# Kernel tuning notes

Hardware: AMD Instinct MI355X
Metric: run time of the kernel (lower is better)

Reference implementation:

```python
import jax, jax.numpy as jnp
import numpy as np
from jax import lax

B, S, F, H, O, U = 512, 168, 12, 128, 3, 256
PERIODS = (3, 6, 12, 24)


def _glorot(key, shape):
    fan_in = shape[-1]
    fan_out = shape[-2] if len(shape) >= 2 else shape[-1]
    scale = jnp.sqrt(2.0 / (fan_in + fan_out))
    return jax.random.normal(key, shape, jnp.float32) * scale


def setup_inputs() -> dict:
    key = jax.random.key(0)
    ks = iter(jax.random.split(key, 64))
    inp = {"x": jax.random.normal(next(ks), (B, 1, F, S), jnp.float32)}
    # 3 SFF groups (group1: enc_in=12, groups 2/3: enc_in=3) share conv/linear shapes per period
    for p in PERIODS:
        k = 1 + 2 * (p // 2)
        inp[f"conv{p}"] = _glorot(next(ks), (3, k))             # [group, kernel]
        inp[f"lin{p}"] = _glorot(next(ks), (3, S // p, S // p))  # [group, seg_y, seg_x]
    inp["Wb0"] = _glorot(next(ks), (U, F + H)); inp["bb0"] = jnp.zeros((U,), jnp.float32)
    inp["Wb1"] = _glorot(next(ks), (U, U));     inp["bb1"] = jnp.zeros((U,), jnp.float32)
    inp["Wff1"] = _glorot(next(ks), (H, U));    inp["bff1"] = jnp.zeros((H,), jnp.float32)
    inp["Wff2"] = _glorot(next(ks), (H, U));    inp["bff2"] = jnp.zeros((H,), jnp.float32)
    inp["Wta"] = _glorot(next(ks), (H, U));     inp["bta"] = jnp.zeros((H,), jnp.float32)
    inp["Wtb"] = _glorot(next(ks), (H, U));     inp["btb"] = jnp.zeros((H,), jnp.float32)
    inp["Wfc"] = _glorot(next(ks), (O, H));     inp["bfc"] = jnp.zeros((O,), jnp.float32)
    inp["Wfits"] = _glorot(next(ks), (O, S, S))  # FF: individual per-channel linear seq->pred
    return inp


def _sff(x, conv_w, lin_w, p):
    # x: [B, S, C]; conv_w: [k]; lin_w: [seg_y, seg_x]
    Bx, Sx, C = x.shape
    xp = jnp.transpose(x, (0, 2, 1))                      # [B, C, S]
    xr = xp.reshape(Bx * C, 1, Sx)
    pad = p // 2
    conv = lax.conv_general_dilated(xr, conv_w.reshape(1, 1, -1), (1,), [(pad, pad)],
                                    dimension_numbers=("NCH", "OIH", "NCH"))
    xc = conv.reshape(Bx, C, Sx) + xp                     # residual smoothing
    seg = Sx // p
    xc = jnp.transpose(xc.reshape(Bx * C, seg, p), (0, 2, 1))  # [B*C, p, seg_x]
    y = jnp.einsum("npk,qk->npq", xc, lin_w)              # [B*C, p, seg_y]
    y = jnp.transpose(y, (0, 2, 1)).reshape(Bx, C, -1)    # [B, C, pred]
    return jnp.transpose(y, (0, 2, 1))                    # [B, pred, C]


def reference(x, conv3, lin3, conv6, lin6, conv12, lin12, conv24, lin24,
              Wb0, bb0, Wb1, bb1, Wff1, bff1, Wff2, bff2,
              Wta, bta, Wtb, btb, Wfc, bfc, Wfits):
    convs = {3: conv3, 6: conv6, 12: conv12, 24: conv24}
    lins = {3: lin3, 6: lin6, 12: lin12, 24: lin24}

    xs = jnp.transpose(x[:, 0], (0, 2, 1))                # [B, S, F]
    seq_mean = jnp.mean(xs, axis=1, keepdims=True)        # [B, 1, F]
    xs = xs - seq_mean

    x1 = sum(_sff(xs, convs[p][0], lins[p][0], p) for p in PERIODS) * 0.25   # [B,S,F]
    xin3 = x1[:, :, :3]
    x2 = sum(_sff(xin3, convs[p][1], lins[p][1], p) for p in PERIODS) * 0.25  # [B,S,3]
    x3 = sum(_sff(xin3, convs[p][2], lins[p][2], p) for p in PERIODS) * 0.25  # [B,S,3]

    # CfC recurrence (ts == 1.0 everywhere; dropout in eval mode = identity)
    def step(h, xt):
        z = jnp.concatenate([xt, h], axis=1)
        z = jax.nn.silu(z @ Wb0.T + bb0)
        z = jax.nn.silu(z @ Wb1.T + bb1)
        ff1 = jnp.tanh(z @ Wff1.T + bff1)
        ff2 = jnp.tanh(z @ Wff2.T + bff2)
        t_interp = jax.nn.sigmoid((z @ Wta.T + bta) + (z @ Wtb.T + btb))
        h_new = ff1 * (1.0 - t_interp) + t_interp * ff2
        return h_new, h_new

    h0 = jnp.zeros((x1.shape[0], Wff1.shape[0]), x1.dtype)
    _, hs = lax.scan(step, h0, jnp.transpose(x1, (1, 0, 2)))  # hs: [S, B, H]

    readout = jnp.einsum("sbh,oh->bso", hs, Wfc) + bfc        # [B, S, O]
    readout = readout + x3
    readout = jnp.einsum("bsc,cps->bpc", readout, Wfits)      # FF (per-channel S -> pred)
    return readout + seq_mean[:, :, :3] + x2
```

## Files before the change

### kernel.cpp

```cpp
#include <hip/hip_runtime.h>

#define BB 512
#define SS 168
#define FF 12
#define HH 128
#define UU 256

typedef unsigned short u16;
typedef unsigned int   u32;
typedef _Float16 f16x8 __attribute__((ext_vector_type(8)));
typedef float    f32x4 __attribute__((ext_vector_type(4)));

__device__ __forceinline__ float sigmoidf_(float x){ return __fdividef(1.f, 1.f + __expf(-x)); }
__device__ __forceinline__ float siluf_(float x){ return x * sigmoidf_(x); }
__device__ __forceinline__ float tanhf_(float x){
    float t = __expf(-2.f * fabsf(x));
    float y = __fdividef(1.f - t, 1.f + t);
    return copysignf(y, x);
}
__device__ __forceinline__ u16 f2h_(float v){ return __builtin_bit_cast(u16, (_Float16)v); }
__device__ __forceinline__ f16x8 bc8_(uint4 v){ return __builtin_bit_cast(f16x8, v); }
__device__ __forceinline__ int aslot_(int row, int k){
    return (k >> 5) * 512 + ((k & 31) >> 3) * 128 + row * 8 + (k & 7);
}

#define MFMA16(a, b, acc) __builtin_amdgcn_mfma_f32_16x16x32_f16((a), (b), (acc), 0, 0, 0)

#define PREP_BLOCKS 810
#define SFFA_BLOCKS (BB * FF)

__global__ __launch_bounds__(256) void front_kernel(
    const float* __restrict__ x,
    const float* __restrict__ c3,  const float* __restrict__ l3,
    const float* __restrict__ c6,  const float* __restrict__ l6,
    const float* __restrict__ c12, const float* __restrict__ l12,
    const float* __restrict__ c24, const float* __restrict__ l24,
    const float* __restrict__ Wb0, const float* __restrict__ Wb1,
    const float* __restrict__ Wff1, const float* __restrict__ Wff2,
    const float* __restrict__ Wta, const float* __restrict__ Wtb,
    const float* __restrict__ Wfc,
    u16* __restrict__ W0f, u16* __restrict__ W1f, u16* __restrict__ W4f,
    float* __restrict__ meanbuf, float* __restrict__ x1,
    float* __restrict__ x2, float* __restrict__ x3)
{
    if (blockIdx.x < PREP_BLOCKS) {
        int t = blockIdx.x * 256 + threadIdx.x;
        if (t < 43520) {
            int e = t & 7, c = (t >> 3) & 15, g = (t >> 7) & 3, rest = t >> 9;
            int s = rest % 5, tt = rest / 5;
            int k = s * 32 + g * 8 + e;
            float v;
            if (tt < 16) { int u = tt * 16 + c; v = (k < 140) ? Wb0[u * 140 + k] : 0.f; }
            else         { v = (c < 3 && k >= 12 && k < 140) ? Wfc[c * 128 + (k - 12)] : 0.f; }
            W0f[t] = f2h_(v);
        } else if (t < 43520 + 65536) {
            int t1 = t - 43520;
            int e = t1 & 7, c = (t1 >> 3) & 15, g = (t1 >> 7) & 3, rest = t1 >> 9;
            int s = rest & 7, tt = rest >> 3;
            int u = tt * 16 + c, k = s * 32 + g * 8 + e;
            W1f[t1] = f2h_(Wb1[u * 256 + k]);
        } else if (t < 43520 + 65536 + 98304) {
            int t2 = t - 109056;
            int e = t2 & 7, c = (t2 >> 3) & 15, g = (t2 >> 7) & 3, rest = t2 >> 9;
            int s = rest & 7, tt = rest >> 3;
            int u = (tt & 7) * 16 + c, k = s * 32 + g * 8 + e;
            float v;
            if      (tt < 8)  v = Wff1[u * 256 + k];
            else if (tt < 16) v = Wff2[u * 256 + k];
            else              v = Wta[u * 256 + k] + Wtb[u * 256 + k];
            W4f[t2] = f2h_(v);
        }
        return;
    }

    int bc = blockIdx.x - PREP_BLOCKS;
    int b = bc / FF, c = bc % FF;
    __shared__ float v[SS], cv[SS], red[256];
    int tid = threadIdx.x;

    float raw = 0.f;
    if (tid < SS) raw = x[(b * FF + c) * SS + tid];
    red[tid] = raw;
    __syncthreads();
    for (int off = 128; off > 0; off >>= 1) {
        if (tid < off) red[tid] += red[tid + off];
        __syncthreads();
    }
    float mv = red[0] * (1.f / SS);
    if (tid == 0) meanbuf[b * FF + c] = mv;
    if (tid < SS) v[tid] = raw - mv;
    __syncthreads();

    const float* cw[4]  = {c3, c6, c12, c24};
    const float* lwv[4] = {l3, l6, l12, l24};
    const int P[4] = {3, 6, 12, 24};
    float acc = 0.f;
    for (int pi = 0; pi < 4; ++pi) {
        int p = P[pi], pad = p >> 1, k = 1 + 2 * pad, seg = SS / p;
        const float* cwp = cw[pi];
        float cc = 0.f;
        if (tid < SS) {
            cc = v[tid];
            for (int j = 0; j < k; ++j) {
                int t = tid + j - pad;
                if (t >= 0 && t < SS) cc += cwp[j] * v[t];
            }
        }
        __syncthreads();
        if (tid < SS) cv[tid] = cc;
        __syncthreads();
        if (tid < SS) {
            int q = tid / p, ph = tid - q * p;
            const float* lwp = lwv[pi];
            float a = 0.f;
            for (int kk = 0; kk < seg; ++kk) a += lwp[q * seg + kk] * cv[kk * p + ph];
            acc += a;
        }
    }
    float x1v = 0.25f * acc;
    if (tid < SS) x1[(b * SS + tid) * FF + c] = x1v;
    if (c >= 3) return;

    __syncthreads();
    if (tid < SS) v[tid] = x1v;
    __syncthreads();
    float acc2 = 0.f, acc3 = 0.f;
    for (int pi = 0; pi < 4; ++pi) {
        int p = P[pi], pad = p >> 1, k = 1 + 2 * pad, seg = SS / p;
        for (int row = 1; row <= 2; ++row) {
            const float* cwp = cw[pi] + row * k;
            float cc = 0.f;
            if (tid < SS) {
                cc = v[tid];
                for (int j = 0; j < k; ++j) {
                    int t = tid + j - pad;
                    if (t >= 0 && t < SS) cc += cwp[j] * v[t];
                }
            }
            __syncthreads();
            if (tid < SS) cv[tid] = cc;
            __syncthreads();
            if (tid < SS) {
                int q = tid / p, ph = tid - q * p;
                const float* lwp = lwv[pi] + row * seg * seg;
                float a = 0.f;
                for (int kk = 0; kk < seg; ++kk) a += lwp[q * seg + kk] * cv[kk * p + ph];
                if (row == 1) acc2 += a; else acc3 += a;
            }
        }
    }
    if (tid < SS) {
        x2[(b * SS + tid) * 3 + c] = 0.25f * acc2;
        x3[(b * SS + tid) * 3 + c] = 0.25f * acc3;
    }
}

__global__ __launch_bounds__(512, 2) void scan_kernel(
    const float* __restrict__ x1g,
    const uint4* __restrict__ W0f, const uint4* __restrict__ W1f, const uint4* __restrict__ W4f,
    const float* __restrict__ bb0, const float* __restrict__ bb1,
    const float* __restrict__ bff1, const float* __restrict__ bff2,
    const float* __restrict__ bta,  const float* __restrict__ btb,
    const float* __restrict__ bfc,
    float* __restrict__ r1g)
{
    const int b0 = blockIdx.x * 4;
    const int tid = threadIdx.x;
    const int w = tid >> 6, lane = tid & 63;
    const int cl = lane & 15, grp = lane >> 4;

    __shared__ __align__(16) u16 W0ro_s[2560];
    __shared__ __align__(16) u16 xh[8064];
    __shared__ __align__(16) u16 zin_s[2560];
    __shared__ __align__(16) u16 z1_s[4096];
    __shared__ __align__(16) u16 z2_s[4096];
    __shared__ __align__(16) float r1s[2016];
    __shared__ float bfcs[4];

    uint4* W0ro4 = (uint4*)W0ro_s;
    uint4* zin4  = (uint4*)zin_s;
    uint4* z1_4  = (uint4*)z1_s;
    uint4* z2_4  = (uint4*)z2_s;

    f16x8 w0a[5], w0b[5];
    f16x8 w1f0[8], w1f1[8], w4a[8], w4b[8], w4c[8];
    #pragma unroll
    for (int s = 0; s < 5; ++s) {
        w0a[s] = bc8_(W0f[((w    ) * 5 + s) * 64 + lane]);
        w0b[s] = bc8_(W0f[((w + 8) * 5 + s) * 64 + lane]);
    }
    #pragma unroll
    for (int s = 0; s < 8; ++s) {
        w1f0[s] = bc8_(W1f[((w     ) * 8 + s) * 64 + lane]);
        w1f1[s] = bc8_(W1f[((w +  8) * 8 + s) * 64 + lane]);
        w4a[s]  = bc8_(W4f[((w     ) * 8 + s) * 64 + lane]);
        w4b[s]  = bc8_(W4f[((w +  8) * 8 + s) * 64 + lane]);
        w4c[s]  = bc8_(W4f[((w + 16) * 8 + s) * 64 + lane]);
    }
    const int u = w * 16 + cl;
    const float bz1a = bb0[u],  bz1b = bb0[128 + u];
    const float bz2a = bb1[u],  bz2b = bb1[128 + u];
    const float bf1r = bff1[u], bf2r = bff2[u];
    const float btsr = bta[u] + btb[u];

    for (int i = tid; i < 320; i += 512) W0ro4[i] = W0f[5120 + i];
    for (int i = tid; i < 8064; i += 512) {
        int s = i / 48, rem = i - s * 48, r = rem / 12, ii = rem - r * 12;
        xh[i] = f2h_(x1g[((b0 + r) * SS + s) * FF + ii]);
    }
    for (int i = tid; i < 320; i += 512) zin4[i] = make_uint4(0, 0, 0, 0);
    for (int i = tid; i < 512; i += 512) z1_4[i] = make_uint4(0, 0, 0, 0);
    for (int i = tid; i < 512; i += 512) z2_4[i] = make_uint4(0, 0, 0, 0);
    if (tid < 3) bfcs[tid] = bfc[tid];
    __syncthreads();
    if (tid < 48) {
        int r = tid / 12, i = tid % 12;
        zin_s[aslot_(r * 4, i)] = xh[tid];
    }
    __syncthreads();

    #pragma unroll 1
    for (int s = 0; s < SS; ++s) {
        f32x4 a1a0 = {0.f,0.f,0.f,0.f}, a1a1 = {0.f,0.f,0.f,0.f};
        f32x4 a1b0 = {0.f,0.f,0.f,0.f}, a1b1 = {0.f,0.f,0.f,0.f};
        f32x4 accr = {0.f,0.f,0.f,0.f};
        #pragma unroll
        for (int ks = 0; ks < 5; ++ks) {
            f16x8 av = bc8_(zin4[ks * 64 + lane]);
            if (ks & 1) { a1a1 = MFMA16(av, w0a[ks], a1a1); a1b1 = MFMA16(av, w0b[ks], a1b1); }
            else        { a1a0 = MFMA16(av, w0a[ks], a1a0); a1b0 = MFMA16(av, w0b[ks], a1b0); }
            if (w == 0) accr = MFMA16(av, bc8_(W0ro4[ks * 64 + lane]), accr);
        }
        if (w == 0 && s > 0 && cl < 3)
            r1s[grp * 504 + (s - 1) * 3 + cl] = accr[0] + bfcs[cl];

        {
            int tr = grp * 4;
            z1_s[aslot_(tr, u)]       = f2h_(siluf_(a1a0[0] + a1a1[0] + bz1a));
            z1_s[aslot_(tr, 128 + u)] = f2h_(siluf_(a1b0[0] + a1b1[0] + bz1b));
        }
        __syncthreads();

        f32x4 a2a0 = {0.f,0.f,0.f,0.f}, a2a1 = {0.f,0.f,0.f,0.f};
        f32x4 a2b0 = {0.f,0.f,0.f,0.f}, a2b1 = {0.f,0.f,0.f,0.f};
        #pragma unroll
        for (int ks = 0; ks < 8; ++ks) {
            f16x8 av = bc8_(z1_4[ks * 64 + lane]);
            if (ks & 1) { a2a1 = MFMA16(av, w1f0[ks], a2a1); a2b1 = MFMA16(av, w1f1[ks], a2b1); }
            else        { a2a0 = MFMA16(av, w1f0[ks], a2a0); a2b0 = MFMA16(av, w1f1[ks], a2b0); }
        }
        {
            int tr = grp * 4;
            z2_s[aslot_(tr, u)]       = f2h_(siluf_(a2a0[0] + a2a1[0] + bz2a));
            z2_s[aslot_(tr, 128 + u)] = f2h_(siluf_(a2b0[0] + a2b1[0] + bz2b));
        }
        __syncthreads();

        f32x4 c3a0 = {0.f,0.f,0.f,0.f}, c3a1 = {0.f,0.f,0.f,0.f};
        f32x4 c3b0 = {0.f,0.f,0.f,0.f}, c3b1 = {0.f,0.f,0.f,0.f};
        f32x4 c3c0 = {0.f,0.f,0.f,0.f}, c3c1 = {0.f,0.f,0.f,0.f};
        #pragma unroll
        for (int ks = 0; ks < 8; ++ks) {
            f16x8 av = bc8_(z2_4[ks * 64 + lane]);
            if (ks & 1) {
                c3a1 = MFMA16(av, w4a[ks], c3a1);
                c3b1 = MFMA16(av, w4b[ks], c3b1);
                c3c1 = MFMA16(av, w4c[ks], c3c1);
            } else {
                c3a0 = MFMA16(av, w4a[ks], c3a0);
                c3b0 = MFMA16(av, w4b[ks], c3b0);
                c3c0 = MFMA16(av, w4c[ks], c3c0);
            }
        }

        {
            float ff1v = tanhf_(c3a0[0] + c3a1[0] + bf1r);
            float ff2v = tanhf_(c3b0[0] + c3b1[0] + bf2r);
            float tv   = sigmoidf_(c3c0[0] + c3c1[0] + btsr);
            float h    = ff1v + tv * (ff2v - ff1v);
            zin_s[aslot_(grp * 4, 12 + u)] = f2h_(h);
        }
        if (tid >= 448 && tid < 496 && s + 1 < SS) {
            int idx = tid - 448;
            int r = idx / 12, i = idx % 12;
            zin_s[aslot_(r * 4, i)] = xh[(s + 1) * 48 + idx];
        }
        __syncthreads();
    }

    if (w == 0) {
        f32x4 accr = {0.f, 0.f, 0.f, 0.f};
        #pragma unroll
        for (int ks = 0; ks < 5; ++ks)
            accr = MFMA16(bc8_(zin4[ks * 64 + lane]),
                          bc8_(W0ro4[ks * 64 + lane]), accr);
        if (cl < 3)
            r1s[grp * 504 + 167 * 3 + cl] = accr[0] + bfcs[cl];
    }
    __syncthreads();
    for (int idx = tid; idx < 2016; idx += 512) {
        int r = idx / 504, rem = idx - r * 504;
        r1g[(b0 + r) * 504 + rem] = r1s[r * 504 + rem];
    }
}

__global__ __launch_bounds__(256) void fits_kernel(
    const float* __restrict__ r1, const float* __restrict__ x3,
    const float* __restrict__ Wfits,
    const float* __restrict__ x2, const float* __restrict__ meanbuf,
    float* __restrict__ out)
{
    int bid = blockIdx.x;
    int bt = bid & 7;
    int rest = bid >> 3;
    int c = rest % 3;
    int pt = rest / 3;
    int b0 = bt * 64, p0 = pt * 28;
    __shared__ float rT[168][65];
    __shared__ float wT[28][168];
    int t = threadIdx.x;
    for (int idx = t; idx < 64 * 168; idx += 256) {
        int b = idx / 168, s = idx - b * 168;
        int gi = ((b0 + b) * 168 + s) * 3 + c;
        rT[s][b] = r1[gi] + x3[gi];
    }
    for (int idx = t; idx < 28 * 168; idx += 256) {
        int p = idx / 168, s = idx - p * 168;
        wT[p][s] = Wfits[(c * 168 + p0 + p) * 168 + s];
    }
    __syncthreads();
    int b = t & 63, pq = t >> 6;
    float acc[7] = {0, 0, 0, 0, 0, 0, 0};
    for (int s = 0; s < 168; ++s) {
        float v = rT[s][b];
        #pragma unroll
        for (int j = 0; j < 7; ++j) acc[j] += v * wT[pq * 7 + j][s];
    }
    float mb = meanbuf[(b0 + b) * 12 + c];
    #pragma unroll
    for (int j = 0; j < 7; ++j) {
        int p = p0 + pq * 7 + j;
        int gi = ((b0 + b) * 168 + p) * 3 + c;
        out[gi] = acc[j] + mb + x2[gi];
    }
}

extern "C" void kernel_launch(void* const* d_in, const int* in_sizes, int n_in,
                              void* d_out, int out_size, void* d_ws, size_t ws_size,
                              hipStream_t stream) {
    const float* x    = (const float*)d_in[0];
    const float* c3   = (const float*)d_in[1];
    const float* l3   = (const float*)d_in[2];
    const float* c6   = (const float*)d_in[3];
    const float* l6   = (const float*)d_in[4];
    const float* c12  = (const float*)d_in[5];
    const float* l12  = (const float*)d_in[6];
    const float* c24  = (const float*)d_in[7];
    const float* l24  = (const float*)d_in[8];
    const float* Wb0  = (const float*)d_in[9];
    const float* bb0  = (const float*)d_in[10];
    const float* Wb1  = (const float*)d_in[11];
    const float* bb1  = (const float*)d_in[12];
    const float* Wff1 = (const float*)d_in[13];
    const float* bff1 = (const float*)d_in[14];
    const float* Wff2 = (const float*)d_in[15];
    const float* bff2 = (const float*)d_in[16];
    const float* Wta  = (const float*)d_in[17];
    const float* bta  = (const float*)d_in[18];
    const float* Wtb  = (const float*)d_in[19];
    const float* btb  = (const float*)d_in[20];
    const float* Wfc  = (const float*)d_in[21];
    const float* bfc  = (const float*)d_in[22];
    const float* Wfits= (const float*)d_in[23];

    float* ws      = (float*)d_ws;
    float* meanbuf = ws;
    float* x1      = meanbuf + 6144;
    float* x2      = x1 + 1032192;
    float* x3      = x2 + 258048;
    float* r1      = x3 + 258048;
    u16*   W0f     = (u16*)(r1 + 258048);
    u16*   W1f     = W0f + 43520;
    u16*   W4f     = W1f + 65536;
    float* out     = (float*)d_out;

    front_kernel<<<PREP_BLOCKS + SFFA_BLOCKS, 256, 0, stream>>>(
        x, c3, l3, c6, l6, c12, l12, c24, l24,
        Wb0, Wb1, Wff1, Wff2, Wta, Wtb, Wfc,
        W0f, W1f, W4f, meanbuf, x1, x2, x3);
    scan_kernel<<<BB / 4, 512, 0, stream>>>(x1,
                                            (const uint4*)W0f, (const uint4*)W1f, (const uint4*)W4f,
                                            bb0, bb1, bff1, bff2, bta, btb, bfc, r1);
    fits_kernel<<<144, 256, 0, stream>>>(r1, x3, Wfits, x2, meanbuf, out);
}
```

Measured before the change: 342.2 us.

## Process one batch row per scan block instead of four

The recurrent scan kernel now gives each block a single batch element instead of packing four rows into the 16-row MFMA tile, launching 512 blocks instead of 128. This spreads the serial 168-step recurrence across more blocks so more compute units run at once. The trade-off is that each block runs full 16x16 MFMAs for one useful row, so total MFMA work and weight register loading grow fourfold, and each step's latency stays the same.

Result: slower. 608.2 us (+77.8%).

```diff
diff --git a/kernel.cpp b/kernel.cpp
--- a/kernel.cpp
+++ b/kernel.cpp
@@ -7,7 +7,6 @@
 #define UU 256
 
 typedef unsigned short u16;
-typedef unsigned int   u32;
 typedef _Float16 f16x8 __attribute__((ext_vector_type(8)));
 typedef float    f32x4 __attribute__((ext_vector_type(4)));
 
@@ -164,17 +163,17 @@
     const float* __restrict__ bfc,
     float* __restrict__ r1g)
 {
-    const int b0 = blockIdx.x * 4;
+    const int b0 = blockIdx.x;
     const int tid = threadIdx.x;
     const int w = tid >> 6, lane = tid & 63;
     const int cl = lane & 15, grp = lane >> 4;
 
     __shared__ __align__(16) u16 W0ro_s[2560];
-    __shared__ __align__(16) u16 xh[8064];
+    __shared__ __align__(16) u16 xh[2016];
     __shared__ __align__(16) u16 zin_s[2560];
     __shared__ __align__(16) u16 z1_s[4096];
     __shared__ __align__(16) u16 z2_s[4096];
-    __shared__ __align__(16) float r1s[2016];
+    __shared__ __align__(16) float r1s[504];
     __shared__ float bfcs[4];
 
     uint4* W0ro4 = (uint4*)W0ro_s;
@@ -204,19 +203,13 @@
     const float btsr = bta[u] + btb[u];
 
     for (int i = tid; i < 320; i += 512) W0ro4[i] = W0f[5120 + i];
-    for (int i = tid; i < 8064; i += 512) {
-        int s = i / 48, rem = i - s * 48, r = rem / 12, ii = rem - r * 12;
-        xh[i] = f2h_(x1g[((b0 + r) * SS + s) * FF + ii]);
-    }
+    for (int i = tid; i < 2016; i += 512) xh[i] = f2h_(x1g[b0 * 2016 + i]);
     for (int i = tid; i < 320; i += 512) zin4[i] = make_uint4(0, 0, 0, 0);
     for (int i = tid; i < 512; i += 512) z1_4[i] = make_uint4(0, 0, 0, 0);
     for (int i = tid; i < 512; i += 512) z2_4[i] = make_uint4(0, 0, 0, 0);
     if (tid < 3) bfcs[tid] = bfc[tid];
     __syncthreads();
-    if (tid < 48) {
-        int r = tid / 12, i = tid % 12;
-        zin_s[aslot_(r * 4, i)] = xh[tid];
-    }
+    if (tid < 12) zin_s[aslot_(0, tid)] = xh[tid];
     __syncthreads();
 
     #pragma unroll 1
@@ -231,13 +224,12 @@
             else        { a1a0 = MFMA16(av, w0a[ks], a1a0); a1b0 = MFMA16(av, w0b[ks], a1b0); }
             if (w == 0) accr = MFMA16(av, bc8_(W0ro4[ks * 64 + lane]), accr);
         }
-        if (w == 0 && s > 0 && cl < 3)
-            r1s[grp * 504 + (s - 1) * 3 + cl] = accr[0] + bfcs[cl];
-
-        {
-            int tr = grp * 4;
-            z1_s[aslot_(tr, u)]       = f2h_(siluf_(a1a0[0] + a1a1[0] + bz1a));
-            z1_s[aslot_(tr, 128 + u)] = f2h_(siluf_(a1b0[0] + a1b1[0] + bz1b));
+        if (w == 0 && s > 0 && grp == 0 && cl < 3)
+            r1s[(s - 1) * 3 + cl] = accr[0] + bfcs[cl];
+
+        if (grp == 0) {
+            z1_s[aslot_(0, u)]       = f2h_(siluf_(a1a0[0] + a1a1[0] + bz1a));
+            z1_s[aslot_(0, 128 + u)] = f2h_(siluf_(a1b0[0] + a1b1[0] + bz1b));
         }
         __syncthreads();
 
@@ -249,10 +241,9 @@
             if (ks & 1) { a2a1 = MFMA16(av, w1f0[ks], a2a1); a2b1 = MFMA16(av, w1f1[ks], a2b1); }
             else        { a2a0 = MFMA16(av, w1f0[ks], a2a0); a2b0 = MFMA16(av, w1f1[ks], a2b0); }
         }
-        {
-            int tr = grp * 4;
-            z2_s[aslot_(tr, u)]       = f2h_(siluf_(a2a0[0] + a2a1[0] + bz2a));
-            z2_s[aslot_(tr, 128 + u)] = f2h_(siluf_(a2b0[0] + a2b1[0] + bz2b));
+        if (grp == 0) {
+            z2_s[aslot_(0, u)]       = f2h_(siluf_(a2a0[0] + a2a1[0] + bz2a));
+            z2_s[aslot_(0, 128 + u)] = f2h_(siluf_(a2b0[0] + a2b1[0] + bz2b));
         }
         __syncthreads();
 
@@ -273,17 +264,16 @@
             }
         }
 
-        {
+        if (grp == 0) {
             float ff1v = tanhf_(c3a0[0] + c3a1[0] + bf1r);
             float ff2v = tanhf_(c3b0[0] + c3b1[0] + bf2r);
             float tv   = sigmoidf_(c3c0[0] + c3c1[0] + btsr);
             float h    = ff1v + tv * (ff2v - ff1v);
-            zin_s[aslot_(grp * 4, 12 + u)] = f2h_(h);
-        }
-        if (tid >= 448 && tid < 496 && s + 1 < SS) {
-            int idx = tid - 448;
-            int r = idx / 12, i = idx % 12;
-            zin_s[aslot_(r * 4, i)] = xh[(s + 1) * 48 + idx];
+            zin_s[aslot_(0, 12 + u)] = f2h_(h);
+        }
+        if (tid >= 448 && tid < 460 && s + 1 < SS) {
+            int i = tid - 448;
+            zin_s[aslot_(0, i)] = xh[(s + 1) * 12 + i];
         }
         __syncthreads();
     }
@@ -294,14 +284,11 @@
         for (int ks = 0; ks < 5; ++ks)
             accr = MFMA16(bc8_(zin4[ks * 64 + lane]),
                           bc8_(W0ro4[ks * 64 + lane]), accr);
-        if (cl < 3)
-            r1s[grp * 504 + 167 * 3 + cl] = accr[0] + bfcs[cl];
-    }
-    __syncthreads();
-    for (int idx = tid; idx < 2016; idx += 512) {
-        int r = idx / 504, rem = idx - r * 504;
-        r1g[(b0 + r) * 504 + rem] = r1s[r * 504 + rem];
-    }
+        if (grp == 0 && cl < 3)
+            r1s[167 * 3 + cl] = accr[0] + bfcs[cl];
+    }
+    __syncthreads();
+    for (int i = tid; i < 504; i += 512) r1g[b0 * 504 + i] = r1s[i];
 }
 
 __global__ __launch_bounds__(256) void fits_kernel(
@@ -388,8 +375,8 @@
         x, c3, l3, c6, l6, c12, l12, c24, l24,
         Wb0, Wb1, Wff1, Wff2, Wta, Wtb, Wfc,
         W0f, W1f, W4f, meanbuf, x1, x2, x3);
-    scan_kernel<<<BB / 4, 512, 0, stream>>>(x1,
-                                            (const uint4*)W0f, (const uint4*)W1f, (const uint4*)W4f,
-                                            bb0, bb1, bff1, bff2, bta, btb, bfc, r1);
+    scan_kernel<<<BB, 512, 0, stream>>>(x1,
+                                        (const uint4*)W0f, (const uint4*)W1f, (const uint4*)W4f,
+                                        bb0, bb1, bff1, bff2, bta, btb, bfc, r1);
     fits_kernel<<<144, 256, 0, stream>>>(r1, x3, Wfits, x2, meanbuf, out);
 }
```

## Split input projection out of scan MFMA and parallelize readout across waves

Applied to the files above, without the earlier changes.

The x-part of the first CfC layer (12 inputs) now runs as scalar FP32 FMAs per lane, computed one step ahead and overlapped with the third GEMM. The recurrent K dimension drops from 160 to 128, so each step needs four MFMA k-slices instead of five. Biases are folded into the accumulator initial values. The readout (Wfc) GEMM moves from wave 0's serial five-MFMA chain into one MFMA on each of four waves, summed through shared memory. The layer-0 hidden weights move from registers into 64KB of LDS, trading register pressure for extra LDS reads every step, and the larger LDS footprint may limit occupancy at two blocks per CU.

After: 401.0 us. 1.17x slower.

```diff
diff --git a/kernel.cpp b/kernel.cpp
--- a/kernel.cpp
+++ b/kernel.cpp
@@ -7,7 +7,6 @@
 #define UU 256
 
 typedef unsigned short u16;
-typedef unsigned int   u32;
 typedef _Float16 f16x8 __attribute__((ext_vector_type(8)));
 typedef float    f32x4 __attribute__((ext_vector_type(4)));
 
@@ -26,7 +25,7 @@
 
 #define MFMA16(a, b, acc) __builtin_amdgcn_mfma_f32_16x16x32_f16((a), (b), (acc), 0, 0, 0)
 
-#define PREP_BLOCKS 810
+#define PREP_BLOCKS 776
 #define SFFA_BLOCKS (BB * FF)
 
 __global__ __launch_bounds__(256) void front_kernel(
@@ -39,36 +38,39 @@
     const float* __restrict__ Wff1, const float* __restrict__ Wff2,
     const float* __restrict__ Wta, const float* __restrict__ Wtb,
     const float* __restrict__ Wfc,
-    u16* __restrict__ W0f, u16* __restrict__ W1f, u16* __restrict__ W4f,
+    u16* __restrict__ W0f, u16* __restrict__ ROf,
+    u16* __restrict__ W1f, u16* __restrict__ W4f,
     float* __restrict__ meanbuf, float* __restrict__ x1,
     float* __restrict__ x2, float* __restrict__ x3)
 {
     if (blockIdx.x < PREP_BLOCKS) {
         int t = blockIdx.x * 256 + threadIdx.x;
-        if (t < 43520) {
+        if (t < 32768) {
             int e = t & 7, c = (t >> 3) & 15, g = (t >> 7) & 3, rest = t >> 9;
-            int s = rest % 5, tt = rest / 5;
-            int k = s * 32 + g * 8 + e;
-            float v;
-            if (tt < 16) { int u = tt * 16 + c; v = (k < 140) ? Wb0[u * 140 + k] : 0.f; }
-            else         { v = (c < 3 && k >= 12 && k < 140) ? Wfc[c * 128 + (k - 12)] : 0.f; }
-            W0f[t] = f2h_(v);
-        } else if (t < 43520 + 65536) {
-            int t1 = t - 43520;
-            int e = t1 & 7, c = (t1 >> 3) & 15, g = (t1 >> 7) & 3, rest = t1 >> 9;
+            int ks = rest & 3, tt = rest >> 2;
+            int u = tt * 16 + c, k = ks * 32 + g * 8 + e;
+            W0f[t] = f2h_(Wb0[u * 140 + 12 + k]);
+        } else if (t < 32768 + 2048) {
+            int t1 = t - 32768;
+            int e = t1 & 7, c = (t1 >> 3) & 15, g = (t1 >> 7) & 3, ks = t1 >> 9;
+            int k = ks * 32 + g * 8 + e;
+            ROf[t1] = f2h_((c < 3) ? Wfc[c * 128 + k] : 0.f);
+        } else if (t < 32768 + 2048 + 65536) {
+            int t2 = t - 34816;
+            int e = t2 & 7, c = (t2 >> 3) & 15, g = (t2 >> 7) & 3, rest = t2 >> 9;
             int s = rest & 7, tt = rest >> 3;
             int u = tt * 16 + c, k = s * 32 + g * 8 + e;
-            W1f[t1] = f2h_(Wb1[u * 256 + k]);
-        } else if (t < 43520 + 65536 + 98304) {
-            int t2 = t - 109056;
-            int e = t2 & 7, c = (t2 >> 3) & 15, g = (t2 >> 7) & 3, rest = t2 >> 9;
+            W1f[t2] = f2h_(Wb1[u * 256 + k]);
+        } else if (t < 198656) {
+            int t3 = t - 100352;
+            int e = t3 & 7, c = (t3 >> 3) & 15, g = (t3 >> 7) & 3, rest = t3 >> 9;
             int s = rest & 7, tt = rest >> 3;
             int u = (tt & 7) * 16 + c, k = s * 32 + g * 8 + e;
             float v;
             if      (tt < 8)  v = Wff1[u * 256 + k];
             else if (tt < 16) v = Wff2[u * 256 + k];
             else              v = Wta[u * 256 + k] + Wtb[u * 256 + k];
-            W4f[t2] = f2h_(v);
+            W4f[t3] = f2h_(v);
         }
         return;
     }
@@ -157,38 +159,35 @@
 
 __global__ __launch_bounds__(512, 2) void scan_kernel(
     const float* __restrict__ x1g,
-    const uint4* __restrict__ W0f, const uint4* __restrict__ W1f, const uint4* __restrict__ W4f,
+    const uint4* __restrict__ W0f, const uint4* __restrict__ ROf,
+    const uint4* __restrict__ W1f, const uint4* __restrict__ W4f,
+    const float* __restrict__ Wb0,
     const float* __restrict__ bb0, const float* __restrict__ bb1,
     const float* __restrict__ bff1, const float* __restrict__ bff2,
     const float* __restrict__ bta,  const float* __restrict__ btb,
     const float* __restrict__ bfc,
     float* __restrict__ r1g)
 {
-    const int b0 = blockIdx.x * 4;
+    const int b0r = blockIdx.x * 4;
     const int tid = threadIdx.x;
     const int w = tid >> 6, lane = tid & 63;
     const int cl = lane & 15, grp = lane >> 4;
 
-    __shared__ __align__(16) u16 W0ro_s[2560];
-    __shared__ __align__(16) u16 xh[8064];
-    __shared__ __align__(16) u16 zin_s[2560];
+    __shared__ __align__(16) u16 W0l_s[32768];
+    __shared__ __align__(16) float xf[8064];
+    __shared__ __align__(16) u16 zin_s[2048];
     __shared__ __align__(16) u16 z1_s[4096];
     __shared__ __align__(16) u16 z2_s[4096];
     __shared__ __align__(16) float r1s[2016];
+    __shared__ float pr[48];
     __shared__ float bfcs[4];
 
-    uint4* W0ro4 = (uint4*)W0ro_s;
-    uint4* zin4  = (uint4*)zin_s;
-    uint4* z1_4  = (uint4*)z1_s;
-    uint4* z2_4  = (uint4*)z2_s;
-
-    f16x8 w0a[5], w0b[5];
+    uint4* W0l4 = (uint4*)W0l_s;
+    uint4* zin4 = (uint4*)zin_s;
+    uint4* z1_4 = (uint4*)z1_s;
+    uint4* z2_4 = (uint4*)z2_s;
+
     f16x8 w1f0[8], w1f1[8], w4a[8], w4b[8], w4c[8];
-    #pragma unroll
-    for (int s = 0; s < 5; ++s) {
-        w0a[s] = bc8_(W0f[((w    ) * 5 + s) * 64 + lane]);
-        w0b[s] = bc8_(W0f[((w + 8) * 5 + s) * 64 + lane]);
-    }
     #pragma unroll
     for (int s = 0; s < 8; ++s) {
         w1f0[s] = bc8_(W1f[((w     ) * 8 + s) * 64 + lane]);
@@ -197,52 +196,72 @@
         w4b[s]  = bc8_(W4f[((w +  8) * 8 + s) * 64 + lane]);
         w4c[s]  = bc8_(W4f[((w + 16) * 8 + s) * 64 + lane]);
     }
+    f16x8 rof = bc8_(ROf[(w & 3) * 64 + lane]);
     const int u = w * 16 + cl;
     const float bz1a = bb0[u],  bz1b = bb0[128 + u];
     const float bz2a = bb1[u],  bz2b = bb1[128 + u];
     const float bf1r = bff1[u], bf2r = bff2[u];
     const float btsr = bta[u] + btb[u];
-
-    for (int i = tid; i < 320; i += 512) W0ro4[i] = W0f[5120 + i];
-    for (int i = tid; i < 8064; i += 512) {
-        int s = i / 48, rem = i - s * 48, r = rem / 12, ii = rem - r * 12;
-        xh[i] = f2h_(x1g[((b0 + r) * SS + s) * FF + ii]);
-    }
-    for (int i = tid; i < 320; i += 512) zin4[i] = make_uint4(0, 0, 0, 0);
+    float w0xa[12], w0xb[12];
+    {
+        const float* pa = &Wb0[u * 140];
+        const float* pb = &Wb0[(128 + u) * 140];
+        #pragma unroll
+        for (int i = 0; i < 12; ++i) { w0xa[i] = pa[i]; w0xb[i] = pb[i]; }
+    }
+
+    for (int i = tid; i < 4096; i += 512) W0l4[i] = W0f[i];
+    for (int i = tid; i < 8064; i += 512) xf[i] = x1g[b0r * 2016 + i];
+    for (int i = tid; i < 256; i += 512) zin4[i] = make_uint4(0, 0, 0, 0);
     for (int i = tid; i < 512; i += 512) z1_4[i] = make_uint4(0, 0, 0, 0);
     for (int i = tid; i < 512; i += 512) z2_4[i] = make_uint4(0, 0, 0, 0);
     if (tid < 3) bfcs[tid] = bfc[tid];
     __syncthreads();
-    if (tid < 48) {
-        int r = tid / 12, i = tid % 12;
-        zin_s[aslot_(r * 4, i)] = xh[tid];
-    }
-    __syncthreads();
+
+    float z1xa, z1xb;
+    {
+        const float4* xr = (const float4*)&xf[grp * 2016];
+        float4 x0 = xr[0], x1v = xr[1], x2v = xr[2];
+        z1xa = w0xa[0]*x0.x + w0xa[1]*x0.y + w0xa[2]*x0.z + w0xa[3]*x0.w
+             + w0xa[4]*x1v.x + w0xa[5]*x1v.y + w0xa[6]*x1v.z + w0xa[7]*x1v.w
+             + w0xa[8]*x2v.x + w0xa[9]*x2v.y + w0xa[10]*x2v.z + w0xa[11]*x2v.w;
+        z1xb = w0xb[0]*x0.x + w0xb[1]*x0.y + w0xb[2]*x0.z + w0xb[3]*x0.w
+             + w0xb[4]*x1v.x + w0xb[5]*x1v.y + w0xb[6]*x1v.z + w0xb[7]*x1v.w
+             + w0xb[8]*x2v.x + w0xb[9]*x2v.y + w0xb[10]*x2v.z + w0xb[11]*x2v.w;
+    }
 
     #pragma unroll 1
     for (int s = 0; s < SS; ++s) {
-        f32x4 a1a0 = {0.f,0.f,0.f,0.f}, a1a1 = {0.f,0.f,0.f,0.f};
-        f32x4 a1b0 = {0.f,0.f,0.f,0.f}, a1b1 = {0.f,0.f,0.f,0.f};
-        f32x4 accr = {0.f,0.f,0.f,0.f};
+        f32x4 a1a0 = {z1xa + bz1a, 0.f, 0.f, 0.f}, a1a1 = {0.f, 0.f, 0.f, 0.f};
+        f32x4 a1b0 = {z1xb + bz1b, 0.f, 0.f, 0.f}, a1b1 = {0.f, 0.f, 0.f, 0.f};
         #pragma unroll
-        for (int ks = 0; ks < 5; ++ks) {
+        for (int ks = 0; ks < 4; ++ks) {
             f16x8 av = bc8_(zin4[ks * 64 + lane]);
-            if (ks & 1) { a1a1 = MFMA16(av, w0a[ks], a1a1); a1b1 = MFMA16(av, w0b[ks], a1b1); }
-            else        { a1a0 = MFMA16(av, w0a[ks], a1a0); a1b0 = MFMA16(av, w0b[ks], a1b0); }
-            if (w == 0) accr = MFMA16(av, bc8_(W0ro4[ks * 64 + lane]), accr);
-        }
-        if (w == 0 && s > 0 && cl < 3)
-            r1s[grp * 504 + (s - 1) * 3 + cl] = accr[0] + bfcs[cl];
-
+            f16x8 b0v = bc8_(W0l4[((w    ) * 4 + ks) * 64 + lane]);
+            f16x8 b1v = bc8_(W0l4[((w + 8) * 4 + ks) * 64 + lane]);
+            if (ks & 1) { a1a1 = MFMA16(av, b0v, a1a1); a1b1 = MFMA16(av, b1v, a1b1); }
+            else        { a1a0 = MFMA16(av, b0v, a1a0); a1b0 = MFMA16(av, b1v, a1b0); }
+        }
+        if (w >= 4) {
+            f32x4 accp = {0.f, 0.f, 0.f, 0.f};
+            accp = MFMA16(bc8_(zin4[(w - 4) * 64 + lane]), rof, accp);
+            if (cl < 3) pr[(w - 4) * 12 + grp * 3 + cl] = accp[0];
+        }
         {
             int tr = grp * 4;
-            z1_s[aslot_(tr, u)]       = f2h_(siluf_(a1a0[0] + a1a1[0] + bz1a));
-            z1_s[aslot_(tr, 128 + u)] = f2h_(siluf_(a1b0[0] + a1b1[0] + bz1b));
-        }
-        __syncthreads();
-
-        f32x4 a2a0 = {0.f,0.f,0.f,0.f}, a2a1 = {0.f,0.f,0.f,0.f};
-        f32x4 a2b0 = {0.f,0.f,0.f,0.f}, a2b1 = {0.f,0.f,0.f,0.f};
+            z1_s[aslot_(tr, u)]       = f2h_(siluf_(a1a0[0] + a1a1[0]));
+            z1_s[aslot_(tr, 128 + u)] = f2h_(siluf_(a1b0[0] + a1b1[0]));
+        }
+        __syncthreads();
+
+        if (s > 0 && tid < 12) {
+            int r = tid / 3, c = tid - r * 3;
+            r1s[r * 504 + (s - 1) * 3 + c] =
+                pr[r * 3 + c] + pr[12 + r * 3 + c] + pr[24 + r * 3 + c] + pr[36 + r * 3 + c]
+                + bfcs[c];
+        }
+        f32x4 a2a0 = {bz2a, 0.f, 0.f, 0.f}, a2a1 = {0.f, 0.f, 0.f, 0.f};
+        f32x4 a2b0 = {bz2b, 0.f, 0.f, 0.f}, a2b1 = {0.f, 0.f, 0.f, 0.f};
         #pragma unroll
         for (int ks = 0; ks < 8; ++ks) {
             f16x8 av = bc8_(z1_4[ks * 64 + lane]);
@@ -251,14 +270,14 @@
         }
         {
             int tr = grp * 4;
-            z2_s[aslot_(tr, u)]       = f2h_(siluf_(a2a0[0] + a2a1[0] + bz2a));
-            z2_s[aslot_(tr, 128 + u)] = f2h_(siluf_(a2b0[0] + a2b1[0] + bz2b));
-        }
-        __syncthreads();
-
-        f32x4 c3a0 = {0.f,0.f,0.f,0.f}, c3a1 = {0.f,0.f,0.f,0.f};
-        f32x4 c3b0 = {0.f,0.f,0.f,0.f}, c3b1 = {0.f,0.f,0.f,0.f};
-        f32x4 c3c0 = {0.f,0.f,0.f,0.f}, c3c1 = {0.f,0.f,0.f,0.f};
+            z2_s[aslot_(tr, u)]       = f2h_(siluf_(a2a0[0] + a2a1[0]));
+            z2_s[aslot_(tr, 128 + u)] = f2h_(siluf_(a2b0[0] + a2b1[0]));
+        }
+        __syncthreads();
+
+        f32x4 c3a0 = {bf1r, 0.f, 0.f, 0.f}, c3a1 = {0.f, 0.f, 0.f, 0.f};
+        f32x4 c3b0 = {bf2r, 0.f, 0.f, 0.f}, c3b1 = {0.f, 0.f, 0.f, 0.f};
+        f32x4 c3c0 = {btsr, 0.f, 0.f, 0.f}, c3c1 = {0.f, 0.f, 0.f, 0.f};
         #pragma unroll
         for (int ks = 0; ks < 8; ++ks) {
             f16x8 av = bc8_(z2_4[ks * 64 + lane]);
@@ -273,34 +292,43 @@
             }
         }
 
+        if (s + 1 < SS) {
+            const float4* xr = (const float4*)&xf[grp * 2016 + (s + 1) * 12];
+            float4 x0 = xr[0], x1v = xr[1], x2v = xr[2];
+            z1xa = w0xa[0]*x0.x + w0xa[1]*x0.y + w0xa[2]*x0.z + w0xa[3]*x0.w
+                 + w0xa[4]*x1v.x + w0xa[5]*x1v.y + w0xa[6]*x1v.z + w0xa[7]*x1v.w
+                 + w0xa[8]*x2v.x + w0xa[9]*x2v.y + w0xa[10]*x2v.z + w0xa[11]*x2v.w;
+            z1xb = w0xb[0]*x0.x + w0xb[1]*x0.y + w0xb[2]*x0.z + w0xb[3]*x0.w
+                 + w0xb[4]*x1v.x + w0xb[5]*x1v.y + w0xb[6]*x1v.z + w0xb[7]*x1v.w
+                 + w0xb[8]*x2v.x + w0xb[9]*x2v.y + w0xb[10]*x2v.z + w0xb[11]*x2v.w;
+        }
+
         {
-            float ff1v = tanhf_(c3a0[0] + c3a1[0] + bf1r);
-            float ff2v = tanhf_(c3b0[0] + c3b1[0] + bf2r);
-            float tv   = sigmoidf_(c3c0[0] + c3c1[0] + btsr);
+            float ff1v = tanhf_(c3a0[0] + c3a1[0]);
+            float ff2v = tanhf_(c3b0[0] + c3b1[0]);
+            float tv   = sigmoidf_(c3c0[0] + c3c1[0]);
             float h    = ff1v + tv * (ff2v - ff1v);
-            zin_s[aslot_(grp * 4, 12 + u)] = f2h_(h);
-        }
-        if (tid >= 448 && tid < 496 && s + 1 < SS) {
-            int idx = tid - 448;
-            int r = idx / 12, i = idx % 12;
-            zin_s[aslot_(r * 4, i)] = xh[(s + 1) * 48 + idx];
-        }
-        __syncthreads();
-    }
-
-    if (w == 0) {
-        f32x4 accr = {0.f, 0.f, 0.f, 0.f};
-        #pragma unroll
-        for (int ks = 0; ks < 5; ++ks)
-            accr = MFMA16(bc8_(zin4[ks * 64 + lane]),
-                          bc8_(W0ro4[ks * 64 + lane]), accr);
-        if (cl < 3)
-            r1s[grp * 504 + 167 * 3 + cl] = accr[0] + bfcs[cl];
-    }
-    __syncthreads();
-    for (int idx = tid; idx < 2016; idx += 512) {
-        int r = idx / 504, rem = idx - r * 504;
-        r1g[(b0 + r) * 504 + rem] = r1s[r * 504 + rem];
+            zin_s[aslot_(grp * 4, u)] = f2h_(h);
+        }
+        __syncthreads();
+    }
+
+    if (w >= 4) {
+        f32x4 accp = {0.f, 0.f, 0.f, 0.f};
+        accp = MFMA16(bc8_(zin4[(w - 4) * 64 + lane]), rof, accp);
+        if (cl < 3) pr[(w - 4) * 12 + grp * 3 + cl] = accp[0];
+    }
+    __syncthreads();
+    if (tid < 12) {
+        int r = tid / 3, c = tid - r * 3;
+        r1s[r * 504 + 167 * 3 + c] =
+            pr[r * 3 + c] + pr[12 + r * 3 + c] + pr[24 + r * 3 + c] + pr[36 + r * 3 + c]
+            + bfcs[c];
+    }
+    __syncthreads();
+    for (int i = tid; i < 2016; i += 512) {
+        int r = i / 504, rem = i - r * 504;
+        r1g[(b0r + r) * 504 + rem] = r1s[i];
     }
 }
 
@@ -380,16 +408,19 @@
     float* x3      = x2 + 258048;
     float* r1      = x3 + 258048;
     u16*   W0f     = (u16*)(r1 + 258048);
-    u16*   W1f     = W0f + 43520;
+    u16*   ROf     = W0f + 32768;
+    u16*   W1f     = ROf + 2048;
     u16*   W4f     = W1f + 65536;
     float* out     = (float*)d_out;
 
     front_kernel<<<PREP_BLOCKS + SFFA_BLOCKS, 256, 0, stream>>>(
         x, c3, l3, c6, l6, c12, l12, c24, l24,
         Wb0, Wb1, Wff1, Wff2, Wta, Wtb, Wfc,
-        W0f, W1f, W4f, meanbuf, x1, x2, x3);
+        W0f, ROf, W1f, W4f, meanbuf, x1, x2, x3);
     scan_kernel<<<BB / 4, 512, 0, stream>>>(x1,
-                                            (const uint4*)W0f, (const uint4*)W1f, (const uint4*)W4f,
+                                            (const uint4*)W0f, (const uint4*)ROf,
+                                            (const uint4*)W1f, (const uint4*)W4f,
+                                            Wb0,
                                             bb0, bb1, bff1, bff2, bta, btb, bfc, r1);
     fits_kernel<<<144, 256, 0, stream>>>(r1, x3, Wfits, x2, meanbuf, out);
 }
```
